# Performance work log

Hardware: AMD Instinct MI355X
Metric: run time of the kernel (lower is better)

The kernel has to match this reference:

```python
import jax, jax.numpy as jnp
import numpy as np

NUM_HEADS = 8

def setup_inputs() -> dict:
    key = jax.random.key(0)
    ks = jax.random.split(key, 6)
    B, nW, F_W, ED = 8, 64, 128, 512
    x = jax.random.normal(ks[0], (B * nW, F_W, ED), dtype=jnp.float32)
    adj_mask = jax.random.normal(ks[1], (B, NUM_HEADS, F_W, F_W), dtype=jnp.float32)
    qkv_w = jax.random.normal(ks[2], (ED, 3 * ED), dtype=jnp.float32) * (ED ** -0.5)
    qkv_b = jax.random.normal(ks[3], (3 * ED,), dtype=jnp.float32) * 0.02
    proj_w = jax.random.normal(ks[4], (ED, ED), dtype=jnp.float32) * (ED ** -0.5)
    proj_b = jax.random.normal(ks[5], (ED,), dtype=jnp.float32) * 0.02
    return {"x": x, "adj_mask": adj_mask, "qkv_w": qkv_w, "qkv_b": qkv_b,
            "proj_w": proj_w, "proj_b": proj_b, "B": B, "nW": nW}

def reference(x, adj_mask, qkv_w, qkv_b, proj_w, proj_b, B, nW):
    B_nW, F_W, ED = x.shape
    H = NUM_HEADS
    hd = ED // H
    scale = hd ** -0.5
    # qkv projection: [B_nW, F_W, 3, H, hd]
    qkv = (x @ qkv_w + qkv_b).reshape(B_nW, F_W, 3, H, hd)
    qkv = jnp.transpose(qkv, (2, 0, 3, 1, 4))  # [3, B_nW, H, F_W, hd]
    q, k, v = qkv[0], qkv[1], qkv[2]
    attn = jnp.einsum('bhqd,bhkd->bhqk', q * scale, k)  # [B_nW, H, F_W, F_W]
    # additive adjacency mask, broadcast over windows
    attn = attn.reshape(B, nW, H, F_W, F_W) + adj_mask[:, None]
    attn = attn.reshape(B_nW, H, F_W, F_W)
    attn = jax.nn.softmax(attn, axis=-1)
    out = jnp.einsum('bhqk,bhkd->bhqd', attn, v)  # [B_nW, H, F_W, hd]
    out = jnp.transpose(out, (0, 2, 1, 3)).reshape(B_nW, F_W, ED)
    return out @ proj_w + proj_b
```

## Files before the change

### kernel.cpp

```cpp
#include <hip/hip_runtime.h>

typedef __bf16 bf16_t;
typedef __bf16 bf16x8 __attribute__((ext_vector_type(8)));
typedef float f32x4 __attribute__((ext_vector_type(4)));

#define MFMA16(a, b, c) __builtin_amdgcn_mfma_f32_16x16x32_bf16(a, b, c, 0, 0, 0)

#define F_W 128
#define ED 512
#define NH 8
#define HD 64
#define B_NW 512

typedef const __attribute__((address_space(1))) void gvoid_t;
typedef __attribute__((address_space(3))) void lvoid_t;
__device__ __forceinline__ void gload16(const void* g, void* l) {
    __builtin_amdgcn_global_load_lds((gvoid_t*)g, (lvoid_t*)l, 16, 0, 0);
}

__global__ __launch_bounds__(256) void prep_kernel(
    const float* __restrict__ qkv_w,
    const float* __restrict__ proj_w,
    bf16_t* __restrict__ qkv_wt,
    bf16_t* __restrict__ proj_wt) {
    int idx = blockIdx.x * 256 + threadIdx.x;
    if (idx < 1536 * 512) {
        int n = idx >> 9, k = idx & 511;
        qkv_wt[idx] = (bf16_t)qkv_w[k * 1536 + n];
    }
    if (idx < 512 * 512) {
        int n = idx >> 9, k = idx & 511;
        proj_wt[idx] = (bf16_t)proj_w[k * 512 + n];
    }
}

__global__ __launch_bounds__(256, 3) void fused_attn_kernel(
    const float* __restrict__ x,
    const float* __restrict__ adj,
    const float* __restrict__ qkv_b,
    const bf16_t* __restrict__ qkv_wt,
    bf16_t* __restrict__ attn_out) {
    __shared__ __align__(16) char smem[49152];
    float*  x_s32  = (float*)smem;
    bf16_t* wt_s   = (bf16_t*)(smem + 16384);
    bf16_t* q_lds  = (bf16_t*)smem;
    bf16_t* k_lds  = (bf16_t*)(smem + 16384);
    bf16_t* p_lds  = (bf16_t*)smem;
    bf16_t* vt_lds = (bf16_t*)(smem + 32768);

    const int tid  = threadIdx.x;
    const int wave = tid >> 6;
    const int lane = tid & 63;
    const int lrow = lane & 15;
    const int lgrp = lane >> 4;
    const int bid = blockIdx.x;
    const int w = (bid & 7) * 64 + (bid >> 6);
    const int h = (bid >> 3) & 7;
    const int bidx = bid & 7;

    const float* xw = x + (size_t)w * F_W * ED;

    const int xrow_l = lane >> 3;
    const int xcol_l = (((lane & 7) * 4) ^ ((xrow_l & 7) << 2));
    const int wrow_l = lane >> 2;
    const int wcol_l = ((((lane & 3) * 8)) ^ ((wrow_l & 3) << 3));

    f32x4 acc[2][12];
#pragma unroll
    for (int mf = 0; mf < 2; ++mf)
#pragma unroll
        for (int nf = 0; nf < 12; ++nf) acc[mf][nf] = (f32x4)0.0f;

    for (int kc = 0; kc < 16; ++kc) {
        const int k0 = kc * 32;
        __syncthreads();
#pragma unroll
        for (int i = 0; i < 4; ++i) {
            int c = wave * 4 + i;
            const float* g = xw + (size_t)(c * 8 + xrow_l) * ED + k0 + xcol_l;
            gload16(g, x_s32 + c * 256);
        }
#pragma unroll
        for (int i = 0; i < 3; ++i) {
            int c = wave * 3 + i;
            int r = c * 16 + wrow_l;
            int n = (r >> 6) * 512 + h * 64 + (r & 63);
            const bf16_t* g = qkv_wt + (size_t)n * 512 + k0 + wcol_l;
            gload16(g, wt_s + c * 512);
        }
        __syncthreads();

        bf16x8 a[2], b[12];
#pragma unroll
        for (int mf = 0; mf < 2; ++mf) {
            int row = wave * 32 + mf * 16 + lrow;
            int sw = (row & 7) << 2;
            const float* px = x_s32 + row * 32;
            f32x4 lo = *(const f32x4*)(px + ((lgrp * 8) ^ sw));
            f32x4 hi = *(const f32x4*)(px + ((lgrp * 8 + 4) ^ sw));
            a[mf] = bf16x8{(bf16_t)lo[0], (bf16_t)lo[1], (bf16_t)lo[2], (bf16_t)lo[3],
                           (bf16_t)hi[0], (bf16_t)hi[1], (bf16_t)hi[2], (bf16_t)hi[3]};
        }
#pragma unroll
        for (int nf = 0; nf < 12; ++nf) {
            int row = nf * 16 + lrow;
            b[nf] = *(const bf16x8*)(wt_s + row * 32 + ((lgrp * 8) ^ ((row & 3) << 3)));
        }
#pragma unroll
        for (int mf = 0; mf < 2; ++mf)
#pragma unroll
            for (int nf = 0; nf < 12; ++nf)
                acc[mf][nf] = MFMA16(a[mf], b[nf], acc[mf][nf]);
    }
    __syncthreads();

#pragma unroll
    for (int mf = 0; mf < 2; ++mf) {
#pragma unroll
        for (int nf = 0; nf < 12; ++nf) {
            int s = nf >> 2;
            int dl = (nf & 3) * 16 + lrow;
            float bias = qkv_b[s * 512 + h * 64 + dl];
#pragma unroll
            for (int j = 0; j < 4; ++j) {
                int row = wave * 32 + mf * 16 + lgrp * 4 + j;
                float val = acc[mf][nf][j] + bias;
                if (s == 0)      q_lds[row * 64 + (dl ^ ((row & 7) << 3))] = (bf16_t)(val * 0.125f);
                else if (s == 1) k_lds[row * 64 + (dl ^ ((row & 7) << 3))] = (bf16_t)val;
                else             vt_lds[dl * 128 + (row ^ ((dl & 15) << 3))] = (bf16_t)val;
            }
        }
    }
    __syncthreads();

    f32x4 sacc[2][8];
#pragma unroll
    for (int mf = 0; mf < 2; ++mf)
#pragma unroll
        for (int nf = 0; nf < 8; ++nf) sacc[mf][nf] = (f32x4)0.0f;

#pragma unroll
    for (int kb = 0; kb < 2; ++kb) {
        bf16x8 a[2], b[8];
#pragma unroll
        for (int mf = 0; mf < 2; ++mf) {
            int row = wave * 32 + mf * 16 + lrow;
            a[mf] = *(const bf16x8*)(q_lds + row * 64 + ((kb * 32 + lgrp * 8) ^ ((row & 7) << 3)));
        }
#pragma unroll
        for (int nf = 0; nf < 8; ++nf) {
            int row = nf * 16 + lrow;
            b[nf] = *(const bf16x8*)(k_lds + row * 64 + ((kb * 32 + lgrp * 8) ^ ((row & 7) << 3)));
        }
#pragma unroll
        for (int mf = 0; mf < 2; ++mf)
#pragma unroll
            for (int nf = 0; nf < 8; ++nf)
                sacc[mf][nf] = MFMA16(a[mf], b[nf], sacc[mf][nf]);
    }

    const float* mbase = adj + ((size_t)(bidx * NH + h)) * F_W * F_W;
#pragma unroll
    for (int mf = 0; mf < 2; ++mf) {
#pragma unroll
        for (int j = 0; j < 4; ++j) {
            int row = wave * 32 + mf * 16 + lgrp * 4 + j;
            const float* mrow = mbase + (size_t)row * F_W;
            float mval[8];
#pragma unroll
            for (int nf = 0; nf < 8; ++nf) mval[nf] = mrow[nf * 16 + lrow];
            float mx = -1e30f;
#pragma unroll
            for (int nf = 0; nf < 8; ++nf) {
                sacc[mf][nf][j] += mval[nf];
                mx = fmaxf(mx, sacc[mf][nf][j]);
            }
#pragma unroll
            for (int d = 1; d < 16; d <<= 1) mx = fmaxf(mx, __shfl_xor(mx, d));
            float sum = 0.f;
#pragma unroll
            for (int nf = 0; nf < 8; ++nf) {
                float p = exp2f((sacc[mf][nf][j] - mx) * 1.44269504f);
                sacc[mf][nf][j] = p;
                sum += p;
            }
#pragma unroll
            for (int d = 1; d < 16; d <<= 1) sum += __shfl_xor(sum, d);
            float r = 1.0f / sum;
#pragma unroll
            for (int nf = 0; nf < 8; ++nf) sacc[mf][nf][j] *= r;
        }
    }
    __syncthreads();
#pragma unroll
    for (int mf = 0; mf < 2; ++mf)
#pragma unroll
        for (int nf = 0; nf < 8; ++nf)
#pragma unroll
            for (int j = 0; j < 4; ++j) {
                int row = wave * 32 + mf * 16 + lgrp * 4 + j;
                int col = nf * 16 + lrow;
                p_lds[row * 128 + (col ^ ((row & 15) << 3))] = (bf16_t)sacc[mf][nf][j];
            }
    __syncthreads();

    f32x4 oacc[2][4];
#pragma unroll
    for (int mf = 0; mf < 2; ++mf)
#pragma unroll
        for (int nf = 0; nf < 4; ++nf) oacc[mf][nf] = (f32x4)0.0f;

#pragma unroll
    for (int kb = 0; kb < 4; ++kb) {
        bf16x8 a[2], b[4];
#pragma unroll
        for (int mf = 0; mf < 2; ++mf) {
            int row = wave * 32 + mf * 16 + lrow;
            a[mf] = *(const bf16x8*)(p_lds + row * 128 + ((kb * 32 + lgrp * 8) ^ ((row & 15) << 3)));
        }
#pragma unroll
        for (int nf = 0; nf < 4; ++nf) {
            int d = nf * 16 + lrow;
            b[nf] = *(const bf16x8*)(vt_lds + d * 128 + ((kb * 32 + lgrp * 8) ^ ((d & 15) << 3)));
        }
#pragma unroll
        for (int mf = 0; mf < 2; ++mf)
#pragma unroll
            for (int nf = 0; nf < 4; ++nf)
                oacc[mf][nf] = MFMA16(a[mf], b[nf], oacc[mf][nf]);
    }

    bf16_t* obase = attn_out + (size_t)w * F_W * ED + h * HD;
#pragma unroll
    for (int mf = 0; mf < 2; ++mf)
#pragma unroll
        for (int nf = 0; nf < 4; ++nf)
#pragma unroll
            for (int j = 0; j < 4; ++j) {
                int row = wave * 32 + mf * 16 + lgrp * 4 + j;
                obase[(size_t)row * ED + nf * 16 + lrow] = (bf16_t)oacc[mf][nf][j];
            }
}

__global__ __launch_bounds__(256) void proj_kernel(
    const bf16_t* __restrict__ a_g,
    const bf16_t* __restrict__ bt_g,
    const float* __restrict__ bias,
    float* __restrict__ out) {
    __shared__ __align__(16) bf16_t sm[8192];
    bf16_t* a_s = sm;
    bf16_t* b_s = sm + 4096;
    const int tid = threadIdx.x;
    const int wave = tid >> 6, lane = tid & 63;
    const int lrow = lane & 15, lgrp = lane >> 4;
    const int bid = blockIdx.x;
    const int mtile = (bid & 7) * 64 + (bid >> 5);
    const int ntile = (bid >> 3) & 3;
    const size_t m0 = (size_t)mtile * 128;
    const int n0 = ntile * 128;
    const int wrow_l = lane >> 2;
    const int wcol_l = ((((lane & 3) * 8)) ^ ((wrow_l & 3) << 3));

    f32x4 acc[2][8];
#pragma unroll
    for (int mf = 0; mf < 2; ++mf)
#pragma unroll
        for (int nf = 0; nf < 8; ++nf) acc[mf][nf] = (f32x4)0.0f;

    for (int kc = 0; kc < 16; ++kc) {
        const int k0 = kc * 32;
        __syncthreads();
#pragma unroll
        for (int i = 0; i < 2; ++i) {
            int c = wave * 2 + i;
            gload16(a_g + (m0 + c * 16 + wrow_l) * 512 + k0 + wcol_l, a_s + c * 512);
            gload16(bt_g + (size_t)(n0 + c * 16 + wrow_l) * 512 + k0 + wcol_l, b_s + c * 512);
        }
        __syncthreads();
        bf16x8 a[2], b[8];
#pragma unroll
        for (int mf = 0; mf < 2; ++mf) {
            int row = wave * 32 + mf * 16 + lrow;
            a[mf] = *(const bf16x8*)(a_s + row * 32 + ((lgrp * 8) ^ ((row & 3) << 3)));
        }
#pragma unroll
        for (int nf = 0; nf < 8; ++nf) {
            int row = nf * 16 + lrow;
            b[nf] = *(const bf16x8*)(b_s + row * 32 + ((lgrp * 8) ^ ((row & 3) << 3)));
        }
#pragma unroll
        for (int mf = 0; mf < 2; ++mf)
#pragma unroll
            for (int nf = 0; nf < 8; ++nf)
                acc[mf][nf] = MFMA16(a[mf], b[nf], acc[mf][nf]);
    }

#pragma unroll
    for (int nf = 0; nf < 8; ++nf) {
        int col = n0 + nf * 16 + lrow;
        float bv = bias[col];
#pragma unroll
        for (int mf = 0; mf < 2; ++mf)
#pragma unroll
            for (int j = 0; j < 4; ++j) {
                size_t row = m0 + wave * 32 + mf * 16 + lgrp * 4 + j;
                out[row * 512 + col] = acc[mf][nf][j] + bv;
            }
    }
}

extern "C" void kernel_launch(void* const* d_in, const int* in_sizes, int n_in,
                              void* d_out, int out_size, void* d_ws, size_t ws_size,
                              hipStream_t stream) {
    const float* x      = (const float*)d_in[0];
    const float* adj    = (const float*)d_in[1];
    const float* qkv_w  = (const float*)d_in[2];
    const float* qkv_b  = (const float*)d_in[3];
    const float* proj_w = (const float*)d_in[4];
    const float* proj_b = (const float*)d_in[5];
    float* out = (float*)d_out;

    bf16_t* attn_out = (bf16_t*)d_ws;
    bf16_t* qkv_wt   = attn_out + (size_t)B_NW * F_W * ED;
    bf16_t* proj_wt  = qkv_wt + 1536 * 512;

    prep_kernel<<<3072, 256, 0, stream>>>(qkv_w, proj_w, qkv_wt, proj_wt);
    fused_attn_kernel<<<B_NW * NH, 256, 0, stream>>>(x, adj, qkv_b, qkv_wt, attn_out);
    proj_kernel<<<(B_NW * F_W / 128) * (ED / 128), 256, 0, stream>>>(attn_out, proj_wt, proj_b, out);
}
```

Before: 336.6 us.

## Double-buffer QKV projection loads, convert x to bf16 in LDS, retile waves

```diff
diff --git a/kernel.cpp b/kernel.cpp
--- a/kernel.cpp
+++ b/kernel.cpp
@@ -11,6 +11,7 @@
 #define NH 8
 #define HD 64
 #define B_NW 512
+#define XB_STRIDE 40
 
 typedef const __attribute__((address_space(1))) void gvoid_t;
 typedef __attribute__((address_space(3))) void lvoid_t;
@@ -41,8 +42,10 @@
     const bf16_t* __restrict__ qkv_wt,
     bf16_t* __restrict__ attn_out) {
     __shared__ __align__(16) char smem[49152];
-    float*  x_s32  = (float*)smem;
-    bf16_t* wt_s   = (bf16_t*)(smem + 16384);
+    bf16_t* xb0 = (bf16_t*)smem;
+    bf16_t* xb1 = (bf16_t*)(smem + 10240);
+    bf16_t* wb0 = (bf16_t*)(smem + 20480);
+    bf16_t* wb1 = (bf16_t*)(smem + 32768);
     bf16_t* q_lds  = (bf16_t*)smem;
     bf16_t* k_lds  = (bf16_t*)(smem + 16384);
     bf16_t* p_lds  = (bf16_t*)smem;
@@ -53,6 +56,8 @@
     const int lane = tid & 63;
     const int lrow = lane & 15;
     const int lgrp = lane >> 4;
+    const int wm = wave >> 1;
+    const int wn = wave & 1;
     const int bid = blockIdx.x;
     const int w = (bid & 7) * 64 + (bid >> 6);
     const int h = (bid >> 3) & 7;
@@ -60,74 +65,115 @@
 
     const float* xw = x + (size_t)w * F_W * ED;
 
-    const int xrow_l = lane >> 3;
-    const int xcol_l = (((lane & 7) * 4) ^ ((xrow_l & 7) << 2));
+    const int xr = tid >> 1;
+    const int xc = (tid & 1) * 16;
     const int wrow_l = lane >> 2;
-    const int wcol_l = ((((lane & 3) * 8)) ^ ((wrow_l & 3) << 3));
-
-    f32x4 acc[2][12];
-#pragma unroll
-    for (int mf = 0; mf < 2; ++mf)
-#pragma unroll
-        for (int nf = 0; nf < 12; ++nf) acc[mf][nf] = (f32x4)0.0f;
-
-    for (int kc = 0; kc < 16; ++kc) {
-        const int k0 = kc * 32;
-        __syncthreads();
-#pragma unroll
-        for (int i = 0; i < 4; ++i) {
-            int c = wave * 4 + i;
-            const float* g = xw + (size_t)(c * 8 + xrow_l) * ED + k0 + xcol_l;
-            gload16(g, x_s32 + c * 256);
-        }
+    const int wcol_l = (((lane & 3) * 8)) ^ ((wrow_l & 3) << 3);
+
+    f32x4 acc[4][6];
+#pragma unroll
+    for (int mf = 0; mf < 4; ++mf)
+#pragma unroll
+        for (int nf = 0; nf < 6; ++nf) acc[mf][nf] = (f32x4)0.0f;
+
+    {
+        const float* px = xw + (size_t)xr * ED + xc;
+        float4 v0 = *(const float4*)(px + 0);
+        float4 v1 = *(const float4*)(px + 4);
+        float4 v2 = *(const float4*)(px + 8);
+        float4 v3 = *(const float4*)(px + 12);
 #pragma unroll
         for (int i = 0; i < 3; ++i) {
             int c = wave * 3 + i;
             int r = c * 16 + wrow_l;
             int n = (r >> 6) * 512 + h * 64 + (r & 63);
-            const bf16_t* g = qkv_wt + (size_t)n * 512 + k0 + wcol_l;
-            gload16(g, wt_s + c * 512);
+            gload16(qkv_wt + (size_t)n * 512 + wcol_l, wb0 + c * 512);
+        }
+        bf16x8 lo = {(bf16_t)v0.x, (bf16_t)v0.y, (bf16_t)v0.z, (bf16_t)v0.w,
+                     (bf16_t)v1.x, (bf16_t)v1.y, (bf16_t)v1.z, (bf16_t)v1.w};
+        bf16x8 hi = {(bf16_t)v2.x, (bf16_t)v2.y, (bf16_t)v2.z, (bf16_t)v2.w,
+                     (bf16_t)v3.x, (bf16_t)v3.y, (bf16_t)v3.z, (bf16_t)v3.w};
+        *(bf16x8*)(xb0 + xr * XB_STRIDE + xc) = lo;
+        *(bf16x8*)(xb0 + xr * XB_STRIDE + xc + 8) = hi;
+    }
+    __syncthreads();
+
+#pragma unroll 2
+    for (int kc = 0; kc < 16; ++kc) {
+        bf16_t* xbc = (kc & 1) ? xb1 : xb0;
+        bf16_t* xbn = (kc & 1) ? xb0 : xb1;
+        bf16_t* wbc = (kc & 1) ? wb1 : wb0;
+        bf16_t* wbn = (kc & 1) ? wb0 : wb1;
+        float4 v0, v1, v2, v3;
+        if (kc < 15) {
+            const int k1 = (kc + 1) * 32;
+            const float* px = xw + (size_t)xr * ED + k1 + xc;
+            v0 = *(const float4*)(px + 0);
+            v1 = *(const float4*)(px + 4);
+            v2 = *(const float4*)(px + 8);
+            v3 = *(const float4*)(px + 12);
+#pragma unroll
+            for (int i = 0; i < 3; ++i) {
+                int c = wave * 3 + i;
+                int r = c * 16 + wrow_l;
+                int n = (r >> 6) * 512 + h * 64 + (r & 63);
+                gload16(qkv_wt + (size_t)n * 512 + k1 + wcol_l, wbn + c * 512);
+            }
+        }
+        bf16x8 a[4], b[6];
+#pragma unroll
+        for (int mf = 0; mf < 4; ++mf) {
+            int row = wm * 64 + mf * 16 + lrow;
+            a[mf] = *(const bf16x8*)(xbc + row * XB_STRIDE + lgrp * 8);
+        }
+#pragma unroll
+        for (int nf = 0; nf < 6; ++nf) {
+            int rw = wn * 96 + nf * 16 + lrow;
+            b[nf] = *(const bf16x8*)(wbc + rw * 32 + ((lgrp * 8) ^ ((rw & 3) << 3)));
+        }
+#pragma unroll
+        for (int mf = 0; mf < 4; ++mf)
+#pragma unroll
+            for (int nf = 0; nf < 6; ++nf)
+                acc[mf][nf] = MFMA16(a[mf], b[nf], acc[mf][nf]);
+        if (kc < 15) {
+            bf16x8 lo = {(bf16_t)v0.x, (bf16_t)v0.y, (bf16_t)v0.z, (bf16_t)v0.w,
+                         (bf16_t)v1.x, (bf16_t)v1.y, (bf16_t)v1.z, (bf16_t)v1.w};
+            bf16x8 hi = {(bf16_t)v2.x, (bf16_t)v2.y, (bf16_t)v2.z, (bf16_t)v2.w,
+                         (bf16_t)v3.x, (bf16_t)v3.y, (bf16_t)v3.z, (bf16_t)v3.w};
+            *(bf16x8*)(xbn + xr * XB_STRIDE + xc) = lo;
+            *(bf16x8*)(xbn + xr * XB_STRIDE + xc + 8) = hi;
         }
         __syncthreads();
-
-        bf16x8 a[2], b[12];
-#pragma unroll
-        for (int mf = 0; mf < 2; ++mf) {
-            int row = wave * 32 + mf * 16 + lrow;
-            int sw = (row & 7) << 2;
-            const float* px = x_s32 + row * 32;
-            f32x4 lo = *(const f32x4*)(px + ((lgrp * 8) ^ sw));
-            f32x4 hi = *(const f32x4*)(px + ((lgrp * 8 + 4) ^ sw));
-            a[mf] = bf16x8{(bf16_t)lo[0], (bf16_t)lo[1], (bf16_t)lo[2], (bf16_t)lo[3],
-                           (bf16_t)hi[0], (bf16_t)hi[1], (bf16_t)hi[2], (bf16_t)hi[3]};
-        }
-#pragma unroll
-        for (int nf = 0; nf < 12; ++nf) {
-            int row = nf * 16 + lrow;
-            b[nf] = *(const bf16x8*)(wt_s + row * 32 + ((lgrp * 8) ^ ((row & 3) << 3)));
-        }
-#pragma unroll
-        for (int mf = 0; mf < 2; ++mf)
-#pragma unroll
-            for (int nf = 0; nf < 12; ++nf)
-                acc[mf][nf] = MFMA16(a[mf], b[nf], acc[mf][nf]);
-    }
-    __syncthreads();
-
-#pragma unroll
-    for (int mf = 0; mf < 2; ++mf) {
-#pragma unroll
-        for (int nf = 0; nf < 12; ++nf) {
-            int s = nf >> 2;
-            int dl = (nf & 3) * 16 + lrow;
-            float bias = qkv_b[s * 512 + h * 64 + dl];
+    }
+
+    const float* mbase = adj + ((size_t)(bidx * NH + h)) * F_W * F_W;
+    float mv[2][4][8];
+#pragma unroll
+    for (int mf = 0; mf < 2; ++mf)
+#pragma unroll
+        for (int j = 0; j < 4; ++j) {
+            int row = wave * 32 + mf * 16 + lgrp * 4 + j;
+            const float* mrow = mbase + (size_t)row * F_W;
+#pragma unroll
+            for (int nf = 0; nf < 8; ++nf) mv[mf][j][nf] = mrow[nf * 16 + lrow];
+        }
+
+#pragma unroll
+    for (int mf = 0; mf < 4; ++mf) {
+#pragma unroll
+        for (int nf = 0; nf < 6; ++nf) {
+            int c = wn * 96 + nf * 16 + lrow;
+            int s = c >> 6;
+            int d = c & 63;
+            float bias = qkv_b[s * 512 + h * 64 + d];
 #pragma unroll
             for (int j = 0; j < 4; ++j) {
-                int row = wave * 32 + mf * 16 + lgrp * 4 + j;
+                int r = wm * 64 + mf * 16 + lgrp * 4 + j;
                 float val = acc[mf][nf][j] + bias;
-                if (s == 0)      q_lds[row * 64 + (dl ^ ((row & 7) << 3))] = (bf16_t)(val * 0.125f);
-                else if (s == 1) k_lds[row * 64 + (dl ^ ((row & 7) << 3))] = (bf16_t)val;
-                else             vt_lds[dl * 128 + (row ^ ((dl & 15) << 3))] = (bf16_t)val;
+                if (s == 0)      q_lds[r * 64 + (d ^ ((r & 7) << 3))] = (bf16_t)(val * 0.125f);
+                else if (s == 1) k_lds[r * 64 + (d ^ ((r & 7) << 3))] = (bf16_t)val;
+                else             vt_lds[d * 128 + (r ^ ((d & 15) << 3))] = (bf16_t)val;
             }
         }
     }
@@ -159,20 +205,14 @@
                 sacc[mf][nf] = MFMA16(a[mf], b[nf], sacc[mf][nf]);
     }
 
-    const float* mbase = adj + ((size_t)(bidx * NH + h)) * F_W * F_W;
 #pragma unroll
     for (int mf = 0; mf < 2; ++mf) {
 #pragma unroll
         for (int j = 0; j < 4; ++j) {
-            int row = wave * 32 + mf * 16 + lgrp * 4 + j;
-            const float* mrow = mbase + (size_t)row * F_W;
-            float mval[8];
-#pragma unroll
-            for (int nf = 0; nf < 8; ++nf) mval[nf] = mrow[nf * 16 + lrow];
             float mx = -1e30f;
 #pragma unroll
             for (int nf = 0; nf < 8; ++nf) {
-                sacc[mf][nf][j] += mval[nf];
+                sacc[mf][nf][j] += mv[mf][j][nf];
                 mx = fmaxf(mx, sacc[mf][nf][j]);
             }
 #pragma unroll
```

New measurement: 365.3 us. 8.5% more time.

## Split fused attention into a standalone QKV GEMM kernel and a separate attention kernel

Applied to the files above, without the earlier changes.

```diff
diff --git a/kernel.cpp b/kernel.cpp
--- a/kernel.cpp
+++ b/kernel.cpp
@@ -11,6 +11,7 @@
 #define NH 8
 #define HD 64
 #define B_NW 512
+#define NTOK 65536
 
 typedef const __attribute__((address_space(1))) void gvoid_t;
 typedef __attribute__((address_space(3))) void lvoid_t;
@@ -34,212 +35,261 @@
     }
 }
 
-__global__ __launch_bounds__(256, 3) void fused_attn_kernel(
+__global__ __launch_bounds__(256, 4) void qkv_gemm_kernel(
     const float* __restrict__ x,
-    const float* __restrict__ adj,
+    const bf16_t* __restrict__ qkv_wt,
     const float* __restrict__ qkv_b,
-    const bf16_t* __restrict__ qkv_wt,
-    bf16_t* __restrict__ attn_out) {
-    __shared__ __align__(16) char smem[49152];
-    float*  x_s32  = (float*)smem;
-    bf16_t* wt_s   = (bf16_t*)(smem + 16384);
-    bf16_t* q_lds  = (bf16_t*)smem;
-    bf16_t* k_lds  = (bf16_t*)(smem + 16384);
-    bf16_t* p_lds  = (bf16_t*)smem;
-    bf16_t* vt_lds = (bf16_t*)(smem + 32768);
-
-    const int tid  = threadIdx.x;
-    const int wave = tid >> 6;
-    const int lane = tid & 63;
-    const int lrow = lane & 15;
-    const int lgrp = lane >> 4;
+    bf16_t* qk_ws,
+    bf16_t* vt_ws) {
+    __shared__ __align__(16) char sm[24576];
+    float*  x_s = (float*)sm;
+    bf16_t* w_s = (bf16_t*)(sm + 16384);
+    bf16_t* tb  = (bf16_t*)sm;
+
+    const int tid = threadIdx.x;
+    const int wave = tid >> 6, lane = tid & 63;
+    const int lrow = lane & 15, lgrp = lane >> 4;
+    const int bid = blockIdx.x;
+    const int idx = bid >> 3;
+    const int mt_l = idx / 12;
+    const int nt = idx - mt_l * 12;
+    const int mtile = (bid & 7) * 64 + mt_l;
+    const size_t m0 = (size_t)mtile * 128;
+    const int n0 = nt * 128;
+
+    const int xrow_l = lane >> 3;
+    const int xcol_l = ((lane & 7) * 4) ^ ((xrow_l & 7) << 2);
+    const int wrow_l = lane >> 2;
+    const int wcol_l = ((lane & 3) * 8) ^ ((wrow_l & 3) << 3);
+
+    f32x4 acc[2][8];
+#pragma unroll
+    for (int mf = 0; mf < 2; ++mf)
+#pragma unroll
+        for (int nf = 0; nf < 8; ++nf) acc[mf][nf] = (f32x4)0.0f;
+
+    for (int kc = 0; kc < 16; ++kc) {
+        const int k0 = kc * 32;
+        __syncthreads();
+#pragma unroll
+        for (int i = 0; i < 4; ++i) {
+            int c = wave * 4 + i;
+            gload16(x + (m0 + c * 8 + xrow_l) * 512 + k0 + xcol_l, x_s + c * 256);
+        }
+#pragma unroll
+        for (int i = 0; i < 2; ++i) {
+            int c = wave * 2 + i;
+            int n = n0 + c * 16 + wrow_l;
+            gload16(qkv_wt + (size_t)n * 512 + k0 + wcol_l, w_s + c * 512);
+        }
+        __syncthreads();
+
+        bf16x8 a[2], b[8];
+#pragma unroll
+        for (int mf = 0; mf < 2; ++mf) {
+            int row = wave * 32 + mf * 16 + lrow;
+            int sw = (row & 7) << 2;
+            const float* px = x_s + row * 32;
+            f32x4 lo = *(const f32x4*)(px + ((lgrp * 8) ^ sw));
+            f32x4 hi = *(const f32x4*)(px + ((lgrp * 8 + 4) ^ sw));
+            a[mf] = bf16x8{(bf16_t)lo[0], (bf16_t)lo[1], (bf16_t)lo[2], (bf16_t)lo[3],
+                           (bf16_t)hi[0], (bf16_t)hi[1], (bf16_t)hi[2], (bf16_t)hi[3]};
+        }
+#pragma unroll
+        for (int nf = 0; nf < 8; ++nf) {
+            int row = nf * 16 + lrow;
+            b[nf] = *(const bf16x8*)(w_s + row * 32 + ((lgrp * 8) ^ ((row & 3) << 3)));
+        }
+#pragma unroll
+        for (int mf = 0; mf < 2; ++mf)
+#pragma unroll
+            for (int nf = 0; nf < 8; ++nf)
+                acc[mf][nf] = MFMA16(a[mf], b[nf], acc[mf][nf]);
+    }
+
+    if (nt < 8) {
+        const float scale = (nt < 4) ? 0.125f : 1.0f;
+#pragma unroll
+        for (int nf = 0; nf < 8; ++nf) {
+            int col = n0 + nf * 16 + lrow;
+            float bv = qkv_b[col];
+#pragma unroll
+            for (int mf = 0; mf < 2; ++mf)
+#pragma unroll
+                for (int j = 0; j < 4; ++j) {
+                    int r = wave * 32 + mf * 16 + lgrp * 4 + j;
+                    qk_ws[(m0 + r) * 1024 + col] =
+                        (bf16_t)((acc[mf][nf][j] + bv) * scale);
+                }
+        }
+    } else {
+#pragma unroll
+        for (int hh = 0; hh < 2; ++hh) {
+            int h = (nt - 8) * 2 + hh;
+            __syncthreads();
+#pragma unroll
+            for (int mf = 0; mf < 2; ++mf)
+#pragma unroll
+                for (int nfl = 0; nfl < 4; ++nfl) {
+                    int nf = hh * 4 + nfl;
+                    int d = nfl * 16 + lrow;
+                    float bv = qkv_b[n0 + hh * 64 + d];
+#pragma unroll
+                    for (int j = 0; j < 4; ++j) {
+                        int r = wave * 32 + mf * 16 + lgrp * 4 + j;
+                        tb[r * 72 + d] = (bf16_t)(acc[mf][nf][j] + bv);
+                    }
+                }
+            __syncthreads();
+            {
+                int d = tid & 63;
+                int kh = tid >> 6;
+                bf16_t* outp = vt_ws + ((size_t)(mtile * 8 + h) * 64 + d) * 128 + kh * 32;
+#pragma unroll
+                for (int o = 0; o < 4; ++o) {
+                    bf16x8 v;
+#pragma unroll
+                    for (int e = 0; e < 8; ++e)
+                        v[e] = tb[(kh * 32 + o * 8 + e) * 72 + d];
+                    *(bf16x8*)(outp + o * 8) = v;
+                }
+            }
+        }
+    }
+}
+
+__global__ __launch_bounds__(512, 4) void attn_kernel(
+    bf16_t* qk_ws,
+    const bf16_t* __restrict__ vt_ws,
+    const float* __restrict__ adj) {
+    __shared__ __align__(16) char sm[32768];
+    bf16_t* k_lds  = (bf16_t*)sm;
+    bf16_t* vt_lds = (bf16_t*)(sm + 16384);
+    bf16_t* pbuf   = (bf16_t*)sm;
+
+    const int tid = threadIdx.x;
+    const int wave = tid >> 6, lane = tid & 63;
+    const int lrow = lane & 15, lgrp = lane >> 4;
     const int bid = blockIdx.x;
     const int w = (bid & 7) * 64 + (bid >> 6);
     const int h = (bid >> 3) & 7;
     const int bidx = bid & 7;
 
-    const float* xw = x + (size_t)w * F_W * ED;
-
-    const int xrow_l = lane >> 3;
-    const int xcol_l = (((lane & 7) * 4) ^ ((xrow_l & 7) << 2));
-    const int wrow_l = lane >> 2;
-    const int wcol_l = ((((lane & 3) * 8)) ^ ((wrow_l & 3) << 3));
-
-    f32x4 acc[2][12];
-#pragma unroll
-    for (int mf = 0; mf < 2; ++mf)
-#pragma unroll
-        for (int nf = 0; nf < 12; ++nf) acc[mf][nf] = (f32x4)0.0f;
-
-    for (int kc = 0; kc < 16; ++kc) {
-        const int k0 = kc * 32;
-        __syncthreads();
-#pragma unroll
-        for (int i = 0; i < 4; ++i) {
-            int c = wave * 4 + i;
-            const float* g = xw + (size_t)(c * 8 + xrow_l) * ED + k0 + xcol_l;
-            gload16(g, x_s32 + c * 256);
-        }
-#pragma unroll
-        for (int i = 0; i < 3; ++i) {
-            int c = wave * 3 + i;
-            int r = c * 16 + wrow_l;
-            int n = (r >> 6) * 512 + h * 64 + (r & 63);
-            const bf16_t* g = qkv_wt + (size_t)n * 512 + k0 + wcol_l;
-            gload16(g, wt_s + c * 512);
-        }
-        __syncthreads();
-
-        bf16x8 a[2], b[12];
-#pragma unroll
-        for (int mf = 0; mf < 2; ++mf) {
-            int row = wave * 32 + mf * 16 + lrow;
-            int sw = (row & 7) << 2;
-            const float* px = x_s32 + row * 32;
-            f32x4 lo = *(const f32x4*)(px + ((lgrp * 8) ^ sw));
-            f32x4 hi = *(const f32x4*)(px + ((lgrp * 8 + 4) ^ sw));
-            a[mf] = bf16x8{(bf16_t)lo[0], (bf16_t)lo[1], (bf16_t)lo[2], (bf16_t)lo[3],
-                           (bf16_t)hi[0], (bf16_t)hi[1], (bf16_t)hi[2], (bf16_t)hi[3]};
-        }
-#pragma unroll
-        for (int nf = 0; nf < 12; ++nf) {
-            int row = nf * 16 + lrow;
-            b[nf] = *(const bf16x8*)(wt_s + row * 32 + ((lgrp * 8) ^ ((row & 3) << 3)));
-        }
-#pragma unroll
-        for (int mf = 0; mf < 2; ++mf)
-#pragma unroll
-            for (int nf = 0; nf < 12; ++nf)
-                acc[mf][nf] = MFMA16(a[mf], b[nf], acc[mf][nf]);
+    bf16_t* qrow = qk_ws + (size_t)w * 128 * 1024;
+
+    {
+        const int krow_l = lane >> 3;
+        const int kcol_l = ((lane & 7) * 8) ^ ((krow_l & 7) << 3);
+#pragma unroll
+        for (int i = 0; i < 2; ++i) {
+            int c = wave * 2 + i;
+            gload16(qrow + (size_t)(c * 8 + krow_l) * 1024 + 512 + h * 64 + kcol_l,
+                    k_lds + c * 512);
+        }
+    }
+    {
+        const bf16_t* vtb = vt_ws + (size_t)(w * 8 + h) * 64 * 128;
+        const int vrow_l = lane >> 4;
+#pragma unroll
+        for (int i = 0; i < 2; ++i) {
+            int c = wave * 2 + i;
+            int d = c * 4 + vrow_l;
+            int vcol = ((lane & 15) * 8) ^ ((d & 7) << 3);
+            gload16(vtb + (size_t)d * 128 + vcol, vt_lds + c * 512);
+        }
+    }
+    bf16x8 aq[2];
+    {
+        int row = wave * 16 + lrow;
+#pragma unroll
+        for (int kb = 0; kb < 2; ++kb)
+            aq[kb] = *(const bf16x8*)(qrow + (size_t)row * 1024 + h * 64 + kb * 32 + lgrp * 8);
     }
     __syncthreads();
 
-#pragma unroll
-    for (int mf = 0; mf < 2; ++mf) {
-#pragma unroll
-        for (int nf = 0; nf < 12; ++nf) {
-            int s = nf >> 2;
-            int dl = (nf & 3) * 16 + lrow;
-            float bias = qkv_b[s * 512 + h * 64 + dl];
-#pragma unroll
-            for (int j = 0; j < 4; ++j) {
-                int row = wave * 32 + mf * 16 + lgrp * 4 + j;
-                float val = acc[mf][nf][j] + bias;
-                if (s == 0)      q_lds[row * 64 + (dl ^ ((row & 7) << 3))] = (bf16_t)(val * 0.125f);
-                else if (s == 1) k_lds[row * 64 + (dl ^ ((row & 7) << 3))] = (bf16_t)val;
-                else             vt_lds[dl * 128 + (row ^ ((dl & 15) << 3))] = (bf16_t)val;
-            }
-        }
-    }
-    __syncthreads();
-
-    f32x4 sacc[2][8];
-#pragma unroll
-    for (int mf = 0; mf < 2; ++mf)
-#pragma unroll
-        for (int nf = 0; nf < 8; ++nf) sacc[mf][nf] = (f32x4)0.0f;
-
+    f32x4 sacc[8];
+#pragma unroll
+    for (int nf = 0; nf < 8; ++nf) sacc[nf] = (f32x4)0.0f;
 #pragma unroll
     for (int kb = 0; kb < 2; ++kb) {
-        bf16x8 a[2], b[8];
-#pragma unroll
-        for (int mf = 0; mf < 2; ++mf) {
-            int row = wave * 32 + mf * 16 + lrow;
-            a[mf] = *(const bf16x8*)(q_lds + row * 64 + ((kb * 32 + lgrp * 8) ^ ((row & 7) << 3)));
-        }
+        bf16x8 b[8];
 #pragma unroll
         for (int nf = 0; nf < 8; ++nf) {
             int row = nf * 16 + lrow;
             b[nf] = *(const bf16x8*)(k_lds + row * 64 + ((kb * 32 + lgrp * 8) ^ ((row & 7) << 3)));
         }
 #pragma unroll
-        for (int mf = 0; mf < 2; ++mf)
-#pragma unroll
-            for (int nf = 0; nf < 8; ++nf)
-                sacc[mf][nf] = MFMA16(a[mf], b[nf], sacc[mf][nf]);
+        for (int nf = 0; nf < 8; ++nf)
+            sacc[nf] = MFMA16(aq[kb], b[nf], sacc[nf]);
     }
 
     const float* mbase = adj + ((size_t)(bidx * NH + h)) * F_W * F_W;
 #pragma unroll
-    for (int mf = 0; mf < 2; ++mf) {
-#pragma unroll
-        for (int j = 0; j < 4; ++j) {
-            int row = wave * 32 + mf * 16 + lgrp * 4 + j;
-            const float* mrow = mbase + (size_t)row * F_W;
-            float mval[8];
-#pragma unroll
-            for (int nf = 0; nf < 8; ++nf) mval[nf] = mrow[nf * 16 + lrow];
-            float mx = -1e30f;
-#pragma unroll
-            for (int nf = 0; nf < 8; ++nf) {
-                sacc[mf][nf][j] += mval[nf];
-                mx = fmaxf(mx, sacc[mf][nf][j]);
+    for (int j = 0; j < 4; ++j) {
+        int row = wave * 16 + lgrp * 4 + j;
+        const float* mrow = mbase + (size_t)row * F_W;
+        float mx = -1e30f;
+#pragma unroll
+        for (int nf = 0; nf < 8; ++nf) {
+            sacc[nf][j] += mrow[nf * 16 + lrow];
+            mx = fmaxf(mx, sacc[nf][j]);
+        }
+#pragma unroll
+        for (int d = 1; d < 16; d <<= 1) mx = fmaxf(mx, __shfl_xor(mx, d));
+        float sum = 0.f;
+#pragma unroll
+        for (int nf = 0; nf < 8; ++nf) {
+            float p = exp2f((sacc[nf][j] - mx) * 1.44269504f);
+            sacc[nf][j] = p;
+            sum += p;
+        }
+#pragma unroll
+        for (int d = 1; d < 16; d <<= 1) sum += __shfl_xor(sum, d);
+        float r = 1.0f / sum;
+#pragma unroll
+        for (int nf = 0; nf < 8; ++nf) sacc[nf][j] *= r;
+    }
+    __syncthreads();
+
+    f32x4 oacc[4];
+#pragma unroll
+    for (int nf = 0; nf < 4; ++nf) oacc[nf] = (f32x4)0.0f;
+
+#pragma unroll
+    for (int kb = 0; kb < 4; ++kb) {
+#pragma unroll
+        for (int nn = 0; nn < 2; ++nn) {
+            int nf = kb * 2 + nn;
+            int kk = nn * 16 + lrow;
+#pragma unroll
+            for (int j = 0; j < 4; ++j) {
+                int r = wave * 16 + lgrp * 4 + j;
+                pbuf[r * 40 + kk] = (bf16_t)(sacc[nf][j]);
             }
-#pragma unroll
-            for (int d = 1; d < 16; d <<= 1) mx = fmaxf(mx, __shfl_xor(mx, d));
-            float sum = 0.f;
-#pragma unroll
-            for (int nf = 0; nf < 8; ++nf) {
-                float p = exp2f((sacc[mf][nf][j] - mx) * 1.44269504f);
-                sacc[mf][nf][j] = p;
-                sum += p;
-            }
-#pragma unroll
-            for (int d = 1; d < 16; d <<= 1) sum += __shfl_xor(sum, d);
-            float r = 1.0f / sum;
-#pragma unroll
-            for (int nf = 0; nf < 8; ++nf) sacc[mf][nf][j] *= r;
-        }
-    }
-    __syncthreads();
-#pragma unroll
-    for (int mf = 0; mf < 2; ++mf)
-#pragma unroll
-        for (int nf = 0; nf < 8; ++nf)
-#pragma unroll
-            for (int j = 0; j < 4; ++j) {
-                int row = wave * 32 + mf * 16 + lgrp * 4 + j;
-                int col = nf * 16 + lrow;
-                p_lds[row * 128 + (col ^ ((row & 15) << 3))] = (bf16_t)sacc[mf][nf][j];
-            }
-    __syncthreads();
-
-    f32x4 oacc[2][4];
-#pragma unroll
-    for (int mf = 0; mf < 2; ++mf)
-#pragma unroll
-        for (int nf = 0; nf < 4; ++nf) oacc[mf][nf] = (f32x4)0.0f;
-
-#pragma unroll
-    for (int kb = 0; kb < 4; ++kb) {
-        bf16x8 a[2], b[4];
-#pragma unroll
-        for (int mf = 0; mf < 2; ++mf) {
-            int row = wave * 32 + mf * 16 + lrow;
-            a[mf] = *(const bf16x8*)(p_lds + row * 128 + ((kb * 32 + lgrp * 8) ^ ((row & 15) << 3)));
-        }
+        }
+        __syncthreads();
+        bf16x8 a = *(const bf16x8*)(pbuf + (wave * 16 + lrow) * 40 + lgrp * 8);
+        bf16x8 b[4];
 #pragma unroll
         for (int nf = 0; nf < 4; ++nf) {
             int d = nf * 16 + lrow;
-            b[nf] = *(const bf16x8*)(vt_lds + d * 128 + ((kb * 32 + lgrp * 8) ^ ((d & 15) << 3)));
-        }
-#pragma unroll
-        for (int mf = 0; mf < 2; ++mf)
-#pragma unroll
-            for (int nf = 0; nf < 4; ++nf)
-                oacc[mf][nf] = MFMA16(a[mf], b[nf], oacc[mf][nf]);
-    }
-
-    bf16_t* obase = attn_out + (size_t)w * F_W * ED + h * HD;
-#pragma unroll
-    for (int mf = 0; mf < 2; ++mf)
+            b[nf] = *(const bf16x8*)(vt_lds + d * 128 + ((kb * 32 + lgrp * 8) ^ ((d & 7) << 3)));
+        }
 #pragma unroll
         for (int nf = 0; nf < 4; ++nf)
-#pragma unroll
-            for (int j = 0; j < 4; ++j) {
-                int row = wave * 32 + mf * 16 + lgrp * 4 + j;
-                obase[(size_t)row * ED + nf * 16 + lrow] = (bf16_t)oacc[mf][nf][j];
-            }
+            oacc[nf] = MFMA16(a, b[nf], oacc[nf]);
+        __syncthreads();
+    }
+
+#pragma unroll
+    for (int nf = 0; nf < 4; ++nf) {
+        int ocol = h * 64 + nf * 16 + lrow;
+#pragma unroll
+        for (int j = 0; j < 4; ++j) {
+            int r = wave * 16 + lgrp * 4 + j;
+            qrow[(size_t)r * 1024 + ocol] = (bf16_t)oacc[nf][j];
+        }
+    }
 }
 
 __global__ __launch_bounds__(256) void proj_kernel(
@@ -247,9 +297,9 @@
     const bf16_t* __restrict__ bt_g,
     const float* __restrict__ bias,
     float* __restrict__ out) {
-    __shared__ __align__(16) bf16_t sm[8192];
-    bf16_t* a_s = sm;
-    bf16_t* b_s = sm + 4096;
+    __shared__ __align__(16) bf16_t sm_[8192];
+    bf16_t* a_s = sm_;
+    bf16_t* b_s = sm_ + 4096;
     const int tid = threadIdx.x;
     const int wave = tid >> 6, lane = tid & 63;
     const int lrow = lane & 15, lgrp = lane >> 4;
@@ -259,7 +309,7 @@
     const size_t m0 = (size_t)mtile * 128;
     const int n0 = ntile * 128;
     const int wrow_l = lane >> 2;
-    const int wcol_l = ((((lane & 3) * 8)) ^ ((wrow_l & 3) << 3));
+    const int wcol_l = ((lane & 3) * 8) ^ ((wrow_l & 3) << 3);
 
     f32x4 acc[2][8];
 #pragma unroll
@@ -273,7 +323,7 @@
 #pragma unroll
         for (int i = 0; i < 2; ++i) {
             int c = wave * 2 + i;
-            gload16(a_g + (m0 + c * 16 + wrow_l) * 512 + k0 + wcol_l, a_s + c * 512);
+            gload16(a_g + (m0 + c * 16 + wrow_l) * 1024 + k0 + wcol_l, a_s + c * 512);
             gload16(bt_g + (size_t)(n0 + c * 16 + wrow_l) * 512 + k0 + wcol_l, b_s + c * 512);
         }
         __syncthreads();
@@ -320,11 +370,13 @@
     const float* proj_b = (const float*)d_in[5];
     float* out = (float*)d_out;
 
-    bf16_t* attn_out = (bf16_t*)d_ws;
-    bf16_t* qkv_wt   = attn_out + (size_t)B_NW * F_W * ED;
-    bf16_t* proj_wt  = qkv_wt + 1536 * 512;
+    bf16_t* qk_ws   = (bf16_t*)d_ws;
+    bf16_t* vt_ws   = qk_ws + (size_t)NTOK * 1024;
+    bf16_t* qkv_wt  = vt_ws + (size_t)4096 * 64 * 128;
+    bf16_t* proj_wt = qkv_wt + 1536 * 512;
 
     prep_kernel<<<3072, 256, 0, stream>>>(qkv_w, proj_w, qkv_wt, proj_wt);
-    fused_attn_kernel<<<B_NW * NH, 256, 0, stream>>>(x, adj, qkv_b, qkv_wt, attn_out);
-    proj_kernel<<<(B_NW * F_W / 128) * (ED / 128), 256, 0, stream>>>(attn_out, proj_wt, proj_b, out);
-}
+    qkv_gemm_kernel<<<6144, 256, 0, stream>>>(x, qkv_wt, qkv_b, qk_ws, vt_ws);
+    attn_kernel<<<4096, 512, 0, stream>>>(qk_ws, vt_ws, adj);
+    proj_kernel<<<2048, 256, 0, stream>>>(qk_ws, proj_wt, proj_b, out);
+}
```

Measured after the change: 330.7 us. About the same (-1.7%).
